# Optimization experiments

Measured on AMD Instinct MI355X. Metric: run time of the kernel, lower is better.

The kernel has to match this reference:

```python
import jax, jax.numpy as jnp
import numpy as np

B, S, D, NH = 2, 2048, 2048, 16
HD = D // NH  # 128


def setup_inputs() -> dict:
    key = jax.random.key(0)
    ks = jax.random.split(key, 7)
    s = 1.0 / np.sqrt(D)
    return {
        "hidden_states": jax.random.normal(ks[0], (B, S, D), dtype=jnp.float32),
        "Wq": jax.random.normal(ks[1], (D, D), dtype=jnp.float32) * s,
        "Wk": jax.random.normal(ks[2], (D, D), dtype=jnp.float32) * s,
        "Wv": jax.random.normal(ks[3], (D, D), dtype=jnp.float32) * s,
        "Wo": jax.random.normal(ks[4], (D, D), dtype=jnp.float32) * s,
        # phase projections: hidden -> num_heads (zero-init in the module; use small
        # random values so the phase path is numerically exercised)
        "Wpq": jax.random.normal(ks[5], (D, NH), dtype=jnp.float32) * 0.02,
        "Wpk": jax.random.normal(ks[6], (D, NH), dtype=jnp.float32) * 0.02,
    }


def reference(hidden_states, Wq, Wk, Wv, Wo, Wpq, Wpk):
    x = hidden_states  # [B,S,D]
    # ---- base_attn: standard causal multi-head self-attention ----
    q = (x @ Wq).reshape(B, S, NH, HD).transpose(0, 2, 1, 3)  # [B,H,S,hd]
    k = (x @ Wk).reshape(B, S, NH, HD).transpose(0, 2, 1, 3)
    v = (x @ Wv).reshape(B, S, NH, HD).transpose(0, 2, 1, 3)
    scores = jnp.einsum("bhqd,bhkd->bhqk", q, k) / np.sqrt(HD)  # [B,H,S,S]
    causal = jnp.tril(jnp.ones((S, S), dtype=bool))
    scores = jnp.where(causal, scores, jnp.float32(-1e9))
    probs = jax.nn.softmax(scores, axis=-1)
    ctx = jnp.einsum("bhqk,bhkd->bhqd", probs, v)  # [B,H,S,hd]
    attn_output = ctx.transpose(0, 2, 1, 3).reshape(B, S, D) @ Wo  # [B,S,D]
    # ---- phase modulation ----
    # original: cos(pq[b,q,None,h] - pk[b,None,k,h]).mean(dims=(k,h))  -> [B,S]
    # identity: cos(a-b) = cos a * cos b + sin a * sin b lets us avoid the
    # [B,S,S,H] tensor; the math is identical.
    pq = x @ Wpq  # [B,S,H]
    pk = x @ Wpk  # [B,S,H]
    Ck = jnp.cos(pk).sum(axis=1)  # [B,H]
    Sk = jnp.sin(pk).sum(axis=1)  # [B,H]
    phase_mod = (jnp.cos(pq) * Ck[:, None, :] + jnp.sin(pq) * Sk[:, None, :]).sum(-1) / (S * NH)  # [B,S]
    return attn_output * (1.0 + 0.1 * phase_mod[..., None])
```

## Files before the change

kernel.cpp:

```cpp
#include <hip/hip_runtime.h>
#include <hip/hip_bf16.h>

typedef __attribute__((ext_vector_type(8))) short short8;
typedef __attribute__((ext_vector_type(4))) float f32x4;
typedef __attribute__((ext_vector_type(16))) float f32x16;
typedef __attribute__((ext_vector_type(4))) int i32x4;
typedef unsigned short u16;

#define S_LEN 2048
#define D_DIM 2048
#define NHEAD 16
#define HDIM 128
#define M_ROWS 4096

#define MFMA(a,b,c) __builtin_amdgcn_mfma_f32_16x16x32_bf16(a,b,c,0,0,0)
#define MFMA32(a,b,c) __builtin_amdgcn_mfma_f32_32x32x16_bf16(a,b,c,0,0,0)

__device__ __forceinline__ u16 f2bf(float f) {
  union { float f; unsigned u; } v; v.f = f;
  unsigned r = v.u + 0x7fffu + ((v.u >> 16) & 1u);
  return (u16)(r >> 16);
}

__device__ __forceinline__ void async16(void* lds, const void* g) {
  __builtin_amdgcn_global_load_lds(
      (const __attribute__((address_space(1))) unsigned*)g,
      (__attribute__((address_space(3))) unsigned*)lds, 16, 0, 0);
}

__device__ __forceinline__ unsigned cvtpk(float lo, float hi) {
  unsigned r;
  asm("v_cvt_pk_bf16_f32 %0, %1, %2" : "=v"(r) : "v"(lo), "v"(hi));
  return r;
}
__device__ __forceinline__ void plswap(unsigned& x, unsigned& y) {
  asm("v_permlane32_swap_b32 %0, %1" : "+v"(x), "+v"(y));
}

__global__ void k_cvt_x(const float* __restrict__ x, u16* __restrict__ xb) {
  int i = blockIdx.x * 256 + threadIdx.x;
  float4 v = reinterpret_cast<const float4*>(x)[i];
  ushort4 o;
  o.x = f2bf(v.x); o.y = f2bf(v.y); o.z = f2bf(v.z); o.w = f2bf(v.w);
  reinterpret_cast<ushort4*>(xb)[i] = o;
}

__global__ void k_cvt_wt(const float* __restrict__ W, u16* __restrict__ Wt) {
  __shared__ u16 tile[32][33];
  int n0 = blockIdx.x * 32, k0 = blockIdx.y * 32;
  int tx = threadIdx.x & 31, ty = threadIdx.x >> 5;
#pragma unroll
  for (int i = 0; i < 4; i++)
    tile[ty + i * 8][tx] = f2bf(W[(size_t)(k0 + ty + i * 8) * D_DIM + n0 + tx]);
  __syncthreads();
#pragma unroll
  for (int i = 0; i < 4; i++)
    Wt[(size_t)(n0 + ty + i * 8) * D_DIM + k0 + tx] = tile[tx][ty + i * 8];
}

__global__ void k_vtrans(const u16* __restrict__ V, u16* __restrict__ Vt) {
  __shared__ u16 tile[32][33];
  int s0 = blockIdx.x * 32, d0 = blockIdx.y * 32, bh = blockIdx.z;
  const u16* Vp = V + (size_t)bh * S_LEN * HDIM;
  u16* Vtp = Vt + (size_t)bh * HDIM * S_LEN;
  int tx = threadIdx.x & 31, ty = threadIdx.x >> 5;
#pragma unroll
  for (int i = 0; i < 4; i++)
    tile[ty + i * 8][tx] = Vp[(size_t)(s0 + ty + i * 8) * HDIM + d0 + tx];
  __syncthreads();
#pragma unroll
  for (int i = 0; i < 4; i++)
    Vtp[(size_t)(d0 + ty + i * 8) * S_LEN + s0 + tx] = tile[tx][ty + i * 8];
}

template <int NFRAG, int MODE>
__global__ __launch_bounds__(512, 2) void k_gemm3(const u16* __restrict__ A,
                                                  const u16* __restrict__ Bt,
                                                  void* __restrict__ outp,
                                                  const float* __restrict__ fac) {
  constexpr int BN = NFRAG * 64;
  constexpr int AUNIT = 16384;
  constexpr int BUNIT = BN * 64;
  constexpr int LPU = 2 + NFRAG / 2;
  __shared__ __align__(16) char lds[4 * (AUNIT + BUNIT)];
  const int m0 = blockIdx.y * 256, n0 = blockIdx.x * BN;
  const int t = threadIdx.x;
  const int w = t >> 6, l = t & 63;
  const int wr = (w >> 2) * 128, wc = (w & 3) * (BN / 4);
  const int lr = l & 15, lq = l >> 4;
  const char* Ab = (const char*)A;
  const char* Bb = (const char*)Bt;

  f32x4 acc[8][NFRAG] = {};

  auto stage_unit = [&](int tt) {
    const int slot = tt & 3;
#pragma unroll
    for (int j = 0; j < 2; j++) {
      const int p = j * 8192 + w * 1024 + l * 16;
      const int row = p >> 6, sl = (p >> 4) & 3;
      async16(lds + slot * AUNIT + p,
              Ab + (size_t)(m0 + row) * 4096 + tt * 64 + ((sl ^ ((row >> 1) & 3)) * 16));
    }
#pragma unroll
    for (int j = 0; j < NFRAG / 2; j++) {
      const int p = j * 8192 + w * 1024 + l * 16;
      const int row = p >> 6, sl = (p >> 4) & 3;
      async16(lds + 4 * AUNIT + slot * BUNIT + p,
              Bb + (size_t)(n0 + row) * 4096 + tt * 64 + ((sl ^ ((row >> 1) & 3)) * 16));
    }
  };

  auto compute = [&](int tt) {
    const int slot = tt & 3;
    const char* Ar = lds + slot * AUNIT;
    const char* Br = lds + 4 * AUNIT + slot * BUNIT;
    short8 af[8], bf[NFRAG];
#pragma unroll
    for (int mi = 0; mi < 8; mi++) {
      const int row = wr + mi * 16 + lr;
      af[mi] = *reinterpret_cast<const short8*>(
          Ar + row * 64 + ((lq ^ ((row >> 1) & 3)) * 16));
    }
#pragma unroll
    for (int ni = 0; ni < NFRAG; ni++) {
      const int row = wc + ni * 16 + lr;
      bf[ni] = *reinterpret_cast<const short8*>(
          Br + row * 64 + ((lq ^ ((row >> 1) & 3)) * 16));
    }
    __builtin_amdgcn_s_setprio(1);
#pragma unroll
    for (int mi = 0; mi < 8; mi++)
#pragma unroll
      for (int ni = 0; ni < NFRAG; ni++)
        acc[mi][ni] = MFMA(af[mi], bf[ni], acc[mi][ni]);
    __builtin_amdgcn_s_setprio(0);
  };

  stage_unit(0);
  stage_unit(1);
  stage_unit(2);

  const int NT = D_DIM / 32;
  for (int tt = 0; tt < NT; tt++) {
    if (tt < NT - 2)
      asm volatile("s_waitcnt vmcnt(%0)" :: "n"(2 * LPU) : "memory");
    else if (tt == NT - 2)
      asm volatile("s_waitcnt vmcnt(%0)" :: "n"(LPU) : "memory");
    else
      asm volatile("s_waitcnt vmcnt(0)" ::: "memory");
    __builtin_amdgcn_s_barrier();
    asm volatile("" ::: "memory");
    if (tt + 3 < NT) stage_unit(tt + 3);
    compute(tt);
  }

#pragma unroll
  for (int mi = 0; mi < 8; mi++) {
#pragma unroll
    for (int ni = 0; ni < NFRAG; ni++) {
#pragma unroll
      for (int r = 0; r < 4; r++) {
        const int row = m0 + wr + mi * 16 + lq * 4 + r;
        const int col = n0 + wc + ni * 16 + lr;
        const float v = acc[mi][ni][r];
        if (MODE == 0) {
          const int mat = col >> 11;
          const int hh = (col >> 7) & 15;
          ((u16*)outp)[(size_t)mat * 8388608 +
                       (((size_t)((row >> 11) * NHEAD + hh)) * S_LEN + (row & 2047)) * HDIM +
                       (col & 127)] = f2bf(v);
        } else {
          ((float*)outp)[(size_t)row * D_DIM + col] = v * (1.0f + 0.1f * fac[row]);
        }
      }
    }
  }
}

__global__ __launch_bounds__(256) void k_phase_proj(const u16* __restrict__ xb,
                                                    const float* __restrict__ Wpq,
                                                    const float* __restrict__ Wpk,
                                                    float* __restrict__ pq,
                                                    float* __restrict__ pk) {
  __shared__ u16 xs[16][136];
  __shared__ float2 ws[128][16];
  const int t = threadIdx.x;
  const int m0 = blockIdx.x * 16;
  const int h = t & 15, r = t >> 4;
  float sq = 0.f, sk = 0.f;
  for (int kc = 0; kc < D_DIM; kc += 128) {
    *reinterpret_cast<short8*>(&xs[t >> 4][(t & 15) * 8]) =
        *reinterpret_cast<const short8*>(
            &xb[(size_t)(m0 + (t >> 4)) * D_DIM + kc + (t & 15) * 8]);
#pragma unroll
    for (int j = 0; j < 8; j++) {
      const int idx = j * 256 + t;
      const int k = idx >> 4, hh = idx & 15;
      ws[k][hh] = make_float2(Wpq[(size_t)(kc + k) * NHEAD + hh],
                              Wpk[(size_t)(kc + k) * NHEAD + hh]);
    }
    __syncthreads();
#pragma unroll
    for (int k8 = 0; k8 < 16; k8++) {
      const short8 x8 = *reinterpret_cast<const short8*>(&xs[r][k8 * 8]);
#pragma unroll
      for (int j = 0; j < 8; j++) {
        union { float f; unsigned u; } c;
        c.u = ((unsigned)(u16)x8[j]) << 16;
        const float2 wv = ws[k8 * 8 + j][h];
        sq += c.f * wv.x;
        sk += c.f * wv.y;
      }
    }
    __syncthreads();
  }
  pq[(size_t)(m0 + r) * NHEAD + h] = sq;
  pk[(size_t)(m0 + r) * NHEAD + h] = sk;
}

__device__ __forceinline__ float wave_sum(float v) {
  v += __shfl_xor(v, 1);  v += __shfl_xor(v, 2);  v += __shfl_xor(v, 4);
  v += __shfl_xor(v, 8);  v += __shfl_xor(v, 16); v += __shfl_xor(v, 32);
  return v;
}

__global__ void k_phase_ck(const float* __restrict__ pk, float* __restrict__ Ck,
                           float* __restrict__ Sk) {
  int bh = blockIdx.x, b = bh >> 4, h = bh & 15;
  float c = 0.f, s = 0.f;
  for (int ss = threadIdx.x; ss < S_LEN; ss += 256) {
    float v = pk[((size_t)b * S_LEN + ss) * NHEAD + h];
    c += cosf(v); s += sinf(v);
  }
  c = wave_sum(c); s = wave_sum(s);
  __shared__ float rc[4], rs[4];
  int wv = threadIdx.x >> 6;
  if ((threadIdx.x & 63) == 0) { rc[wv] = c; rs[wv] = s; }
  __syncthreads();
  if (threadIdx.x == 0) {
    Ck[bh] = rc[0] + rc[1] + rc[2] + rc[3];
    Sk[bh] = rs[0] + rs[1] + rs[2] + rs[3];
  }
}

__global__ void k_phase_mod(const float* __restrict__ pq, const float* __restrict__ Ck,
                            const float* __restrict__ Sk, float* __restrict__ pm) {
  int m = blockIdx.x * 256 + threadIdx.x;
  int b = m >> 11;
  float a = 0.f;
#pragma unroll
  for (int h = 0; h < NHEAD; h++) {
    float v = pq[(size_t)m * NHEAD + h];
    a += cosf(v) * Ck[b * NHEAD + h] + sinf(v) * Sk[b * NHEAD + h];
  }
  pm[m] = a * (1.0f / (S_LEN * NHEAD));
}

__global__ __launch_bounds__(256, 2) void k_attn(const u16* __restrict__ Q,
                                                 const u16* __restrict__ K,
                                                 const u16* __restrict__ Vt,
                                                 u16* __restrict__ ctx) {
  const int bh = blockIdx.x;
  const int gy = blockIdx.y;
  const int g = (gy < 8) ? (15 - gy) : (gy - 8);
  const int b = bh >> 4, h = bh & 15;
  const int t = threadIdx.x;
  const int w = t >> 6, l = t & 63;
  const int ln = l & 31, hi = l >> 5;
  const int q0w = g * 128 + w * 32;
  const int qq = q0w + ln;
  const float scale = 0.08838834764831845f;

  const u16* Qp = Q + (size_t)bh * S_LEN * HDIM;
  const char* Kg = (const char*)(K + (size_t)bh * S_LEN * HDIM);
  const char* Vg = (const char*)(Vt + (size_t)bh * HDIM * S_LEN);

  __shared__ __align__(16) char Ks[2][16384];
  __shared__ __align__(16) char Vs[2][16384];

  auto stage = [&](int t64, int buf) {
    const int k0 = t64 * 64;
#pragma unroll
    for (int i = 0; i < 4; i++) {
      const int key = i * 16 + w * 4 + (l >> 4);
      async16(Ks[buf] + i * 4096 + w * 1024,
              Kg + (size_t)(k0 + key) * 256 + (((l & 15) * 16) ^ ((key & 15) << 4)));
      const int d = i * 32 + w * 8 + (l >> 3);
      async16(Vs[buf] + i * 4096 + w * 1024,
              Vg + (size_t)d * (S_LEN * 2) + k0 * 2 + (((l & 7) * 16) ^ ((d & 7) << 4)));
    }
  };

  short8 qf[8];
#pragma unroll
  for (int c = 0; c < 8; c++)
    qf[c] = *reinterpret_cast<const short8*>(Qp + (size_t)qq * HDIM + c * 16 + hi * 8);

  f32x16 o[4];
#pragma unroll
  for (int ds = 0; ds < 4; ds++)
#pragma unroll
    for (int r = 0; r < 16; r++) o[ds][r] = 0.f;
  float mrun = -1e30f, lsum = 0.f;

  const int nt = (g + 1) * 2;
  stage(0, 0);
  for (int t64 = 0; t64 < nt; t64++) {
    const int buf = t64 & 1;
    const int k0 = t64 * 64;
    asm volatile("s_waitcnt vmcnt(0)" ::: "memory");
    __syncthreads();
    if (t64 + 1 < nt) stage(t64 + 1, buf ^ 1);
    if (k0 < q0w + 32) {
      f32x16 s[2];
#pragma unroll
      for (int ks = 0; ks < 2; ks++)
#pragma unroll
        for (int r = 0; r < 16; r++) s[ks][r] = 0.f;
      __builtin_amdgcn_s_setprio(1);
#pragma unroll
      for (int ks = 0; ks < 2; ks++) {
        const int key = ks * 32 + ln;
        const char* kb = Ks[buf] + key * 256;
        const unsigned swzk = (unsigned)((key & 15) << 4);
#pragma unroll
        for (int c = 0; c < 8; c++) {
          const short8 kf = *reinterpret_cast<const short8*>(
              kb + (((unsigned)(c * 32 + hi * 16)) ^ swzk));
          s[ks] = MFMA32(kf, qf[c], s[ks]);
        }
      }
      __builtin_amdgcn_s_setprio(0);
      float p[32];
      float mx = -1e30f;
#pragma unroll
      for (int ks = 0; ks < 2; ks++)
#pragma unroll
        for (int r = 0; r < 16; r++) {
          const int key = k0 + ks * 32 + (r & 3) + 8 * (r >> 2) + 4 * hi;
          const float v = (key <= qq) ? s[ks][r] * scale : -1e30f;
          p[ks * 16 + r] = v;
          mx = fmaxf(mx, v);
        }
      mx = fmaxf(mx, __shfl_xor(mx, 32));
      const float nm = fmaxf(mrun, mx);
      const float f = __expf(mrun - nm);
      float rs = 0.f;
#pragma unroll
      for (int i = 0; i < 32; i++) { p[i] = __expf(p[i] - nm); rs += p[i]; }
      rs += __shfl_xor(rs, 32);
      lsum = lsum * f + rs;
      mrun = nm;
#pragma unroll
      for (int ds = 0; ds < 4; ds++)
#pragma unroll
        for (int r = 0; r < 16; r++) o[ds][r] *= f;
      short8 bfr[4];
#pragma unroll
      for (int sub = 0; sub < 2; sub++) {
#pragma unroll
        for (int half = 0; half < 2; half++) {
          const int pb = sub * 16 + half * 8;
          unsigned X1 = cvtpk(p[pb + 0], p[pb + 1]);
          unsigned X2 = cvtpk(p[pb + 2], p[pb + 3]);
          unsigned Y1 = cvtpk(p[pb + 4], p[pb + 5]);
          unsigned Y2 = cvtpk(p[pb + 6], p[pb + 7]);
          plswap(X1, Y1);
          plswap(X2, Y2);
          i32x4 bw;
          bw[0] = (int)X1; bw[1] = (int)X2; bw[2] = (int)Y1; bw[3] = (int)Y2;
          bfr[sub * 2 + half] = __builtin_bit_cast(short8, bw);
        }
      }
      __builtin_amdgcn_s_setprio(1);
#pragma unroll
      for (int ds = 0; ds < 4; ds++) {
        const int d = ds * 32 + ln;
        const char* vb = Vs[buf] + d * 128;
        const unsigned swzv = (unsigned)((d & 7) << 4);
#pragma unroll
        for (int slot = 0; slot < 4; slot++) {
          const short8 vf = *reinterpret_cast<const short8*>(
              vb + (((unsigned)(slot * 32 + hi * 16)) ^ swzv));
          o[ds] = MFMA32(vf, bfr[slot], o[ds]);
        }
      }
      __builtin_amdgcn_s_setprio(0);
    }
  }

  const float rl = 1.0f / lsum;
#pragma unroll
  for (int ds = 0; ds < 4; ds++) {
#pragma unroll
    for (int rq = 0; rq < 4; rq++) {
      const int d = ds * 32 + 8 * rq + 4 * hi;
      ushort4 pk4;
      pk4.x = f2bf(o[ds][rq * 4 + 0] * rl);
      pk4.y = f2bf(o[ds][rq * 4 + 1] * rl);
      pk4.z = f2bf(o[ds][rq * 4 + 2] * rl);
      pk4.w = f2bf(o[ds][rq * 4 + 3] * rl);
      *reinterpret_cast<ushort4*>(ctx + ((size_t)(b * S_LEN + qq)) * D_DIM + h * HDIM + d) = pk4;
    }
  }
}

extern "C" void kernel_launch(void* const* d_in, const int* in_sizes, int n_in,
                              void* d_out, int out_size, void* d_ws, size_t ws_size,
                              hipStream_t stream) {
  const float* x   = (const float*)d_in[0];
  const float* Wq  = (const float*)d_in[1];
  const float* Wk  = (const float*)d_in[2];
  const float* Wv  = (const float*)d_in[3];
  const float* Wo  = (const float*)d_in[4];
  const float* Wpq = (const float*)d_in[5];
  const float* Wpk = (const float*)d_in[6];

  char* ws = (char*)d_ws;
  u16* xb   = (u16*)(ws + 0);
  u16* Wqt  = (u16*)(ws + 16777216);
  u16* Wkt  = (u16*)(ws + 25165824);
  u16* Wvt  = (u16*)(ws + 33554432);
  u16* Wot  = (u16*)(ws + 41943040);
  u16* Qb   = (u16*)(ws + 50331648);
  u16* Kb   = (u16*)(ws + 67108864);
  u16* Vb   = (u16*)(ws + 83886080);
  u16* Vt   = (u16*)(ws + 100663296);
  float* pq = (float*)(ws + 117440512);
  float* pk = (float*)(ws + 117702656);
  float* Ck = (float*)(ws + 117964800);
  float* Sk = (float*)(ws + 117964928);
  float* pm = (float*)(ws + 117965056);

  k_cvt_x<<<dim3(M_ROWS * D_DIM / 1024), 256, 0, stream>>>(x, xb);
  k_cvt_wt<<<dim3(64, 64), 256, 0, stream>>>(Wq, Wqt);
  k_cvt_wt<<<dim3(64, 64), 256, 0, stream>>>(Wk, Wkt);
  k_cvt_wt<<<dim3(64, 64), 256, 0, stream>>>(Wv, Wvt);
  k_cvt_wt<<<dim3(64, 64), 256, 0, stream>>>(Wo, Wot);

  k_gemm3<4, 0><<<dim3(24, 16), 512, 0, stream>>>(xb, Wqt, Qb, nullptr);

  k_vtrans<<<dim3(64, 4, 32), 256, 0, stream>>>(Vb, Vt);

  k_phase_proj<<<dim3(256), 256, 0, stream>>>(xb, Wpq, Wpk, pq, pk);
  k_phase_ck<<<dim3(32), 256, 0, stream>>>(pk, Ck, Sk);
  k_phase_mod<<<dim3(16), 256, 0, stream>>>(pq, Ck, Sk, pm);

  k_attn<<<dim3(32, 16), 256, 0, stream>>>(Qb, Kb, Vt, Vb );

  k_gemm3<2, 1><<<dim3(16, 16), 512, 0, stream>>>(Vb , Wot, (void*)d_out, pm);
}
```

Baseline: 355.3 us.

## Restructure GEMM pipeline into double-buffered two-phase K steps with wider N tiles

Replaces the 4-slot, 3-deep-prefetch GEMM pipeline with a double buffer. Each buffer holds a 64-wide K chunk split into two sub-stages, with the next chunk's halves prefetched while the current halves compute. N tiles grow (NFRAG 4→6 for QKV, 2→4 for output), so there are fewer blocks and more reuse of each A tile. This lowers prefetch depth and raises register and LDS use per block, which may hurt occupancy or latency hiding. The larger tiles also give fewer blocks for the GPU's CUs (256 and 128).

```diff
diff --git a/kernel.cpp b/kernel.cpp
--- a/kernel.cpp
+++ b/kernel.cpp
@@ -74,15 +74,16 @@
 }
 
 template <int NFRAG, int MODE>
-__global__ __launch_bounds__(512, 2) void k_gemm3(const u16* __restrict__ A,
-                                                  const u16* __restrict__ Bt,
-                                                  void* __restrict__ outp,
-                                                  const float* __restrict__ fac) {
+__global__ __launch_bounds__(512, 2) void k_gemm2p(const u16* __restrict__ A,
+                                                   const u16* __restrict__ Bt,
+                                                   void* __restrict__ outp,
+                                                   const float* __restrict__ fac) {
   constexpr int BN = NFRAG * 64;
-  constexpr int AUNIT = 16384;
-  constexpr int BUNIT = BN * 64;
+  constexpr int ASUB = 16384;
+  constexpr int BSUB = BN * 64;
+  constexpr int BBASE = 4 * ASUB;
   constexpr int LPU = 2 + NFRAG / 2;
-  __shared__ __align__(16) char lds[4 * (AUNIT + BUNIT)];
+  __shared__ __align__(16) char lds[4 * ASUB + 4 * BSUB];
   const int m0 = blockIdx.y * 256, n0 = blockIdx.x * BN;
   const int t = threadIdx.x;
   const int w = t >> 6, l = t & 63;
@@ -93,28 +94,28 @@
 
   f32x4 acc[8][NFRAG] = {};
 
-  auto stage_unit = [&](int tt) {
-    const int slot = tt & 3;
+  auto stage_unit = [&](int tt, int s, int buf) {
 #pragma unroll
     for (int j = 0; j < 2; j++) {
       const int p = j * 8192 + w * 1024 + l * 16;
-      const int row = p >> 6, sl = (p >> 4) & 3;
-      async16(lds + slot * AUNIT + p,
-              Ab + (size_t)(m0 + row) * 4096 + tt * 64 + ((sl ^ ((row >> 1) & 3)) * 16));
+      const int row = p >> 6, slot = (p >> 4) & 3;
+      async16(lds + buf * 2 * ASUB + s * ASUB + j * 8192 + w * 1024,
+              Ab + (size_t)(m0 + row) * 4096 + tt * 128 + s * 64 +
+                  ((slot ^ ((row >> 1) & 3)) * 16));
     }
 #pragma unroll
     for (int j = 0; j < NFRAG / 2; j++) {
       const int p = j * 8192 + w * 1024 + l * 16;
-      const int row = p >> 6, sl = (p >> 4) & 3;
-      async16(lds + 4 * AUNIT + slot * BUNIT + p,
-              Bb + (size_t)(n0 + row) * 4096 + tt * 64 + ((sl ^ ((row >> 1) & 3)) * 16));
+      const int row = p >> 6, slot = (p >> 4) & 3;
+      async16(lds + BBASE + buf * 2 * BSUB + s * BSUB + j * 8192 + w * 1024,
+              Bb + (size_t)(n0 + row) * 4096 + tt * 128 + s * 64 +
+                  ((slot ^ ((row >> 1) & 3)) * 16));
     }
   };
 
-  auto compute = [&](int tt) {
-    const int slot = tt & 3;
-    const char* Ar = lds + slot * AUNIT;
-    const char* Br = lds + 4 * AUNIT + slot * BUNIT;
+  auto phase = [&](int buf, int s) {
+    const char* Ar = lds + buf * 2 * ASUB + s * ASUB;
+    const char* Br = lds + BBASE + buf * 2 * BSUB + s * BSUB;
     short8 af[8], bf[NFRAG];
 #pragma unroll
     for (int mi = 0; mi < 8; mi++) {
@@ -137,22 +138,24 @@
     __builtin_amdgcn_s_setprio(0);
   };
 
-  stage_unit(0);
-  stage_unit(1);
-  stage_unit(2);
-
-  const int NT = D_DIM / 32;
+  stage_unit(0, 0, 0);
+  stage_unit(0, 1, 0);
+
+  const int NT = D_DIM / 64;
   for (int tt = 0; tt < NT; tt++) {
-    if (tt < NT - 2)
-      asm volatile("s_waitcnt vmcnt(%0)" :: "n"(2 * LPU) : "memory");
-    else if (tt == NT - 2)
-      asm volatile("s_waitcnt vmcnt(%0)" :: "n"(LPU) : "memory");
-    else
-      asm volatile("s_waitcnt vmcnt(0)" ::: "memory");
+    const int buf = tt & 1;
+    const bool pf = (tt + 1 < NT);
+    asm volatile("s_waitcnt vmcnt(%0)" :: "n"(LPU) : "memory");
     __builtin_amdgcn_s_barrier();
     asm volatile("" ::: "memory");
-    if (tt + 3 < NT) stage_unit(tt + 3);
-    compute(tt);
+    if (pf) stage_unit(tt + 1, 0, buf ^ 1);
+    phase(buf, 0);
+    if (pf) asm volatile("s_waitcnt vmcnt(%0)" :: "n"(LPU) : "memory");
+    else    asm volatile("s_waitcnt vmcnt(0)" ::: "memory");
+    __builtin_amdgcn_s_barrier();
+    asm volatile("" ::: "memory");
+    if (pf) stage_unit(tt + 1, 1, buf ^ 1);
+    phase(buf, 1);
   }
 
 #pragma unroll
@@ -439,7 +442,7 @@
   k_cvt_wt<<<dim3(64, 64), 256, 0, stream>>>(Wv, Wvt);
   k_cvt_wt<<<dim3(64, 64), 256, 0, stream>>>(Wo, Wot);
 
-  k_gemm3<4, 0><<<dim3(24, 16), 512, 0, stream>>>(xb, Wqt, Qb, nullptr);
+  k_gemm2p<6, 0><<<dim3(16, 16), 512, 0, stream>>>(xb, Wqt, Qb, nullptr);
 
   k_vtrans<<<dim3(64, 4, 32), 256, 0, stream>>>(Vb, Vt);
 
@@ -449,5 +452,5 @@
 
   k_attn<<<dim3(32, 16), 256, 0, stream>>>(Qb, Kb, Vt, Vb );
 
-  k_gemm3<2, 1><<<dim3(16, 16), 512, 0, stream>>>(Vb , Wot, (void*)d_out, pm);
-}
+  k_gemm2p<4, 1><<<dim3(8, 16), 512, 0, stream>>>(Vb , Wot, (void*)d_out, pm);
+}
```

Result: slower. 398.2 us (+12.1%).
